# Performance work log

Measured on AMD Instinct MI355X. Metric: run time of the kernel, lower is better.

The kernel has to match this reference:

```python
import jax, jax.numpy as jnp
import numpy as np
import math

B, L, S, D = 4, 4096, 4096, 256
EPS = 1e-5

def _layernorm(x, g, b):
    mu = jnp.mean(x, axis=-1, keepdims=True)
    var = jnp.mean(jnp.square(x - mu), axis=-1, keepdims=True)
    return (x - mu) * jax.lax.rsqrt(var + EPS) * g + b

def setup_inputs() -> dict:
    key = jax.random.key(0)
    ks = jax.random.split(key, 14)
    s = 1.0 / math.sqrt(D)
    s2 = 1.0 / math.sqrt(2 * D)
    inp = {
        "source": jax.random.normal(ks[0], (B, L, D), jnp.float32),
        "target": jax.random.normal(ks[1], (B, S, D), jnp.float32),
        # linear weights stored as [in, out]
        "Wq": jax.random.uniform(ks[2], (D, D), jnp.float32, -s, s),
        "bq": jnp.zeros((D,), jnp.float32),
        "Wk": jax.random.uniform(ks[3], (D, D), jnp.float32, -s, s),
        "bk": jnp.zeros((D,), jnp.float32),
        "Wv": jax.random.uniform(ks[4], (D, D), jnp.float32, -s, s),
        "bv": jnp.zeros((D,), jnp.float32),
        "Wm": jax.random.uniform(ks[5], (D, D), jnp.float32, -s, s),
        "bm": jnp.zeros((D,), jnp.float32),
        "g1": jnp.ones((D,), jnp.float32),
        "beta1": jnp.zeros((D,), jnp.float32),
        "W1": jax.random.uniform(ks[6], (2 * D, 2 * D), jnp.float32, -s2, s2),
        "W2": jax.random.uniform(ks[7], (2 * D, D), jnp.float32, -s2, s2),
        "g2": jnp.ones((D,), jnp.float32),
        "beta2": jnp.zeros((D,), jnp.float32),
    }
    return inp

def reference(source, target, Wq, bq, Wk, bk, Wv, bv, Wm, bm, g1, beta1, W1, W2, g2, beta2):
    q = source @ Wq + bq              # [B, L, D]
    k = target @ Wk + bk              # [B, S, D]
    v = target @ Wv + bv              # [B, S, D]
    scale = 1.0 / math.sqrt(D)
    scores = jnp.einsum("bld,bsd->bls", q, k) * scale   # [B, L, S] materialized, as in source
    attn = jax.nn.softmax(scores, axis=-1)
    message = jnp.einsum("bls,bsd->bld", attn, v)        # [B, L, D]
    message = message @ Wm + bm
    message = _layernorm(message, g1, beta1)
    h = jnp.concatenate([source, message], axis=-1)      # [B, L, 2D]
    h = jax.nn.gelu(h @ W1, approximate=False)           # torch GELU is exact erf
    message = _layernorm(h @ W2, g2, beta2)
    return source + message
```

## Files before the change

### kernel.cpp

```cpp
#include <hip/hip_runtime.h>

typedef __bf16 bf16x8 __attribute__((ext_vector_type(8)));
typedef float f32x16 __attribute__((ext_vector_type(16)));
typedef float f32x4 __attribute__((ext_vector_type(4)));
typedef unsigned int u32;
typedef unsigned int u32x4 __attribute__((ext_vector_type(4)));
typedef unsigned short u16;
typedef unsigned short u16x4 __attribute__((ext_vector_type(4)));
typedef unsigned short u16x8 __attribute__((ext_vector_type(8)));

#define DEV static __device__ __forceinline__
#define AS1 __attribute__((address_space(1)))
#define AS3 __attribute__((address_space(3)))

DEV u16 f2bf(float f){
  unsigned u = __float_as_uint(f);
  u += 0x7FFFu + ((u >> 16) & 1u);
  return (u16)(u >> 16);
}
DEV float bf2f(u16 h){ return __uint_as_float(((u32)h) << 16); }

DEV void stage16(const u16* gsrc, const u16* ldst){
  __builtin_amdgcn_global_load_lds((const AS1 u32*)(unsigned long long)gsrc,
                                   (AS3 u32*)(u32)(unsigned long long)ldst,
                                   16, 0, 0);
}

constexpr int BATCH = 4, LQ = 4096, SK = 4096, DH = 256, BL = BATCH * LQ;
constexpr int NHALF = 2;
constexpr int ITERS = SK / NHALF / 64;

__global__ void prep_weights(const float* __restrict__ Wq, const float* __restrict__ Wk,
                             const float* __restrict__ Wv, const float* __restrict__ Wm,
                             const float* __restrict__ W1, const float* __restrict__ W2,
                             const float* __restrict__ bk, const float* __restrict__ bv,
                             u16* __restrict__ WqT, u16* __restrict__ WkvT,
                             u16* __restrict__ WmT,
                             u16* __restrict__ W1T, u16* __restrict__ W2T,
                             float* __restrict__ bkv){
  int idx = blockIdx.x * 256 + threadIdx.x;
  if (idx < 262144){
    int which = idx >> 16, i2 = idx & 65535;
    int r = i2 >> 8, c = i2 & 255;
    const float* S = (which==0)?Wq:(which==1)?Wk:(which==2)?Wv:Wm;
    u16*         D = (which==0)?WqT:(which==1)?WkvT:(which==2)?(WkvT+65536):WmT;
    D[c*256 + r] = f2bf(S[i2]);
  } else if (idx < 524288){
    int i2 = idx - 262144;
    int r = i2 >> 9, c = i2 & 511;
    W1T[c*512 + r] = f2bf(W1[i2]);
  } else if (idx < 655360){
    int i2 = idx - 524288;
    int r = i2 >> 8, c = i2 & 255;
    W2T[(size_t)c*512 + r] = f2bf(W2[i2]);
  } else if (idx < 655872){
    int i2 = idx - 655360;
    bkv[i2] = (i2 < 256) ? bk[i2] : bv[i2 - 256];
  }
}

__global__ __launch_bounds__(256, 2) void qkv_gemm(
  const float* __restrict__ src, const float* __restrict__ tgt,
  const u16* __restrict__ WqT, const u16* __restrict__ WkvT,
  const float* __restrict__ bq, const float* __restrict__ bkv,
  u16* __restrict__ qbuf, u16* __restrict__ kbuf, u16* __restrict__ vtbuf,
  u16* __restrict__ hcat, float qscale)
{
  __shared__ u16 A_lds[128 * 64];
  __shared__ u16 B_lds[128 * 64];
  const int tid = threadIdx.x, lane = tid & 63, wid = tid >> 6;
  const int ql = lane & 31, g = lane >> 5;
  const bool isQ = blockIdx.x < 2;
  const int m0 = blockIdx.y * 128;
  const int n0 = (isQ ? blockIdx.x : (blockIdx.x - 2)) * 128;
  const int mr = (wid & 1) * 64, nr = (wid >> 1) * 64;
  const float* Af = isQ ? src : tgt;
  const u16* BTp = isQ ? WqT : WkvT;
  const float* bias = isQ ? bq : bkv;
  const bool wh = isQ && (blockIdx.x == 0);

  f32x16 acc[2][2] = {};
  f32x4 afreg[8];
  u32x4 breg[4];

#define QK_LOAD_A(kb) do { \
    _Pragma("unroll") \
    for (int i = 0; i < 8; i++){ int item = tid + i*256; int r = item>>4, c = (item&15)*4; \
      afreg[i] = *(const f32x4*)&Af[(size_t)(m0+r)*256 + (kb)*64 + c]; } \
  } while(0)
#define QK_LOAD_B(kb) do { \
    _Pragma("unroll") \
    for (int i = 0; i < 4; i++){ int item = tid + i*256; int r = item>>3, c = (item&7)*8; \
      breg[i] = *(const u32x4*)&BTp[(size_t)(n0+r)*256 + (kb)*64 + c]; } \
  } while(0)

  QK_LOAD_A(0); QK_LOAD_B(0);

  for (int kb = 0; kb < 4; ++kb){
    __syncthreads();
    #pragma unroll
    for (int i = 0; i < 8; i++){ int item = tid + i*256; int r = item>>4, c = (item&15)*4;
      u16x4 h; h[0]=f2bf(afreg[i][0]); h[1]=f2bf(afreg[i][1]);
               h[2]=f2bf(afreg[i][2]); h[3]=f2bf(afreg[i][3]);
      *(u16x4*)&A_lds[r*64 + (c ^ ((r&7)*8))] = h;
      if (wh) *(u16x4*)&hcat[(size_t)(m0+r)*512 + kb*64 + c] = h;
    }
    #pragma unroll
    for (int i = 0; i < 4; i++){ int item = tid + i*256; int r = item>>3, c = (item&7)*8;
      *(u32x4*)&B_lds[r*64 + (c ^ ((r&7)*8))] = breg[i]; }
    __syncthreads();
    if (kb + 1 < 4){ QK_LOAD_A(kb+1); QK_LOAD_B(kb+1); }

    #pragma unroll
    for (int kk = 0; kk < 4; kk++){
      bf16x8 af[2], bf[2];
      #pragma unroll
      for (int mi = 0; mi < 2; mi++)
        af[mi] = __builtin_bit_cast(bf16x8,
          *(const u32x4*)&A_lds[(mr+mi*32+ql)*64 + ((kk*16+g*8) ^ ((ql&7)*8))]);
      #pragma unroll
      for (int ni = 0; ni < 2; ni++)
        bf[ni] = __builtin_bit_cast(bf16x8,
          *(const u32x4*)&B_lds[(nr+ni*32+ql)*64 + ((kk*16+g*8) ^ ((ql&7)*8))]);
      #pragma unroll
      for (int mi = 0; mi < 2; mi++)
        #pragma unroll
        for (int ni = 0; ni < 2; ni++)
          acc[mi][ni] = __builtin_amdgcn_mfma_f32_32x32x16_bf16(af[mi], bf[ni], acc[mi][ni], 0, 0, 0);
    }
  }

  #pragma unroll
  for (int mi = 0; mi < 2; mi++){
    #pragma unroll
    for (int ni = 0; ni < 2; ni++){
      const int col = n0 + nr + ni*32 + ql;
      const float bv = bias[col];
      if (isQ){
        #pragma unroll
        for (int j = 0; j < 16; j++){
          int row = m0 + mr + mi*32 + (j&3) + 8*(j>>2) + 4*g;
          qbuf[(size_t)row*256 + col] = f2bf((acc[mi][ni][j] + bv) * qscale);
        }
      } else if (col < 256){
        #pragma unroll
        for (int j = 0; j < 16; j++){
          int row = m0 + mr + mi*32 + (j&3) + 8*(j>>2) + 4*g;
          kbuf[(size_t)row*256 + col] = f2bf(acc[mi][ni][j] + bv);
        }
      } else {
        const int col2 = col - 256;
        #pragma unroll
        for (int qd = 0; qd < 4; qd++){
          u16x4 h;
          #pragma unroll
          for (int i = 0; i < 4; i++) h[i] = f2bf(acc[mi][ni][qd*4+i] + bv);
          int row0 = m0 + mr + mi*32 + qd*8 + 4*g;
          int bb = row0 >> 12, ss = row0 & 4095;
          *(u16x4*)&vtbuf[((size_t)bb*DH + col2)*SK + ss] = h;
        }
      }
    }
  }
}

__global__ __launch_bounds__(512, 2) void gemm_ln_wm(
  const u16* __restrict__ opart, const float* __restrict__ stats,
  const u16* __restrict__ BTp, const float* __restrict__ bias,
  const float* __restrict__ gamma, const float* __restrict__ beta,
  u16* __restrict__ outp)
{
  __shared__ __align__(16) char smem[65792];
  u16* A_lds = (u16*)smem;
  u16* B_lds = (u16*)(smem + 8192);
  float* scratch = (float*)smem;

  const int tid = threadIdx.x, lane = tid & 63, wid = tid >> 6;
  const int ql = lane & 31, g = lane >> 5;
  const int m0 = blockIdx.x * 64;
  const int ar = tid >> 3, ac = (tid & 7) * 8;

  float winv;
  { int row = m0 + ar;
    winv = 1.f / (stats[row] + stats[(size_t)BL + row]); }

  f32x16 acc[2] = {};
  u32x4 areg, areg2;
  u32x4 breg[4];

#define WM_LOAD_A(kb) do { \
    areg  = *(const u32x4*)&opart[(size_t)(m0+ar)*DH + (kb)*64 + ac]; \
    areg2 = *(const u32x4*)&opart[(size_t)BL*DH + (size_t)(m0+ar)*DH + (kb)*64 + ac]; \
  } while(0)
#define WM_LOAD_B(kb) do { \
    _Pragma("unroll") \
    for (int i = 0; i < 4; i++){ int item = tid + i*512; int r = item>>3, c = (item&7)*8; \
      breg[i] = *(const u32x4*)&BTp[(size_t)r*256 + (kb)*64 + c]; } \
  } while(0)

  WM_LOAD_A(0); WM_LOAD_B(0);

  for (int kb = 0; kb < 4; ++kb){
    __syncthreads();
    { u16x8 h;
      #pragma unroll
      for (int e = 0; e < 8; e++){
        u16 h0 = (u16)(areg[e>>1]  >> ((e&1)*16));
        u16 h1 = (u16)(areg2[e>>1] >> ((e&1)*16));
        h[e] = f2bf((bf2f(h0) + bf2f(h1)) * winv);
      }
      *(u16x8*)&A_lds[ar*64 + (ac ^ ((ar&7)*8))] = h; }
    #pragma unroll
    for (int i = 0; i < 4; i++){ int item = tid + i*512; int r = item>>3, c = (item&7)*8;
      *(u32x4*)&B_lds[r*64 + (c ^ ((r&7)*8))] = breg[i]; }
    __syncthreads();
    if (kb + 1 < 4){ WM_LOAD_A(kb+1); WM_LOAD_B(kb+1); }

    #pragma unroll
    for (int kk = 0; kk < 4; kk++){
      bf16x8 af[2];
      #pragma unroll
      for (int mi = 0; mi < 2; mi++)
        af[mi] = __builtin_bit_cast(bf16x8,
          *(const u32x4*)&A_lds[(mi*32+ql)*64 + ((kk*16+g*8) ^ ((ql&7)*8))]);
      bf16x8 bf = __builtin_bit_cast(bf16x8,
        *(const u32x4*)&B_lds[(wid*32+ql)*64 + ((kk*16+g*8) ^ ((ql&7)*8))]);
      #pragma unroll
      for (int mi = 0; mi < 2; mi++)
        acc[mi] = __builtin_amdgcn_mfma_f32_32x32x16_bf16(af[mi], bf, acc[mi], 0, 0, 0);
    }
  }

  __syncthreads();

  const float bv = bias[wid*32 + ql];
  #pragma unroll
  for (int mi = 0; mi < 2; mi++)
    #pragma unroll
    for (int j = 0; j < 16; j++){
      int row = mi*32 + (j&3) + 8*(j>>2) + 4*g;
      scratch[row*257 + wid*32 + ql] = acc[mi][j] + bv;
    }
  __syncthreads();

  f32x4 gv = *(const f32x4*)&gamma[lane*4];
  f32x4 bvv = *(const f32x4*)&beta[lane*4];
  #pragma unroll
  for (int rr = 0; rr < 8; rr++){
    const int row = wid*8 + rr;
    f32x4 v = *(const f32x4*)&scratch[row*257 + lane*4];
    float s1 = v[0]+v[1]+v[2]+v[3];
    float s2 = v[0]*v[0]+v[1]*v[1]+v[2]*v[2]+v[3]*v[3];
    #pragma unroll
    for (int m = 1; m < 64; m <<= 1){ s1 += __shfl_xor(s1, m, 64); s2 += __shfl_xor(s2, m, 64); }
    float mu = s1 * (1.f/DH);
    float var = s2 * (1.f/DH) - mu*mu;
    float rstd = rsqrtf(var + 1e-5f);
    u16x4 h;
    #pragma unroll
    for (int i = 0; i < 4; i++) h[i] = f2bf((v[i]-mu)*rstd*gv[i] + bvv[i]);
    *(u16x4*)&outp[(size_t)(m0+row)*512 + 256 + lane*4] = h;
  }
}

__global__ __launch_bounds__(512, 2) void fused_mlp(
  const u16* __restrict__ hcat, const u16* __restrict__ W1T,
  const u16* __restrict__ W2T, const float* __restrict__ gamma,
  const float* __restrict__ beta, const float* __restrict__ src,
  float* __restrict__ outp)
{
  __shared__ __align__(16) char smem[98304];
  u16* A1 = (u16*)smem;
  u16* B1 = (u16*)(smem + 8192);
  u16* Hl = (u16*)smem;
  u16* B2 = (u16*)(smem + 65536);
  float* scratch = (float*)smem;

  const int tid = threadIdx.x, lane = tid & 63, wid = tid >> 6;
  const int ql = lane & 31, g = lane >> 5;
  const int m0 = blockIdx.x * 64;

  f32x16 acc1[2][2] = {};
  for (int kb = 0; kb < 8; ++kb){
    if (kb) __syncthreads();
    { int r = tid >> 3, slot = tid & 7;
      stage16(&hcat[(size_t)(m0+r)*512 + kb*64 + ((slot ^ (r&7))<<3)],
              &A1[tid*8]); }
    #pragma unroll
    for (int i = 0; i < 8; i++){
      int grp = tid + i*512; int r = grp>>3, slot = grp&7;
      stage16(&W1T[(size_t)r*512 + kb*64 + ((slot ^ (r&7))<<3)], &B1[grp*8]);
    }
    __syncthreads();
    #pragma unroll
    for (int kk = 0; kk < 4; kk++){
      bf16x8 af[2];
      #pragma unroll
      for (int mi = 0; mi < 2; mi++)
        af[mi] = __builtin_bit_cast(bf16x8,
          *(const u32x4*)&A1[(mi*32+ql)*64 + ((kk*16+g*8) ^ ((ql&7)*8))]);
      #pragma unroll
      for (int ni = 0; ni < 2; ni++){
        int rB = wid*64 + ni*32 + ql;
        bf16x8 bf = __builtin_bit_cast(bf16x8,
          *(const u32x4*)&B1[rB*64 + ((kk*16+g*8) ^ ((ql&7)*8))]);
        #pragma unroll
        for (int mi = 0; mi < 2; mi++)
          acc1[mi][ni] = __builtin_amdgcn_mfma_f32_32x32x16_bf16(af[mi], bf, acc1[mi][ni], 0, 0, 0);
      }
    }
  }
  __syncthreads();

  #pragma unroll
  for (int mi = 0; mi < 2; mi++)
    #pragma unroll
    for (int ni = 0; ni < 2; ni++){
      const int col = wid*64 + ni*32 + ql;
      const int s = col >> 3;
      #pragma unroll
      for (int j = 0; j < 16; j++){
        int row = mi*32 + (j&3) + 8*(j>>2) + 4*g;
        float v = acc1[mi][ni][j];
        v = 0.5f * v * (1.f + erff(v * 0.70710678118f));
        Hl[row*512 + ((s ^ (row&7))<<3) + (col&7)] = f2bf(v);
      }
    }
  __syncthreads();

  f32x16 acc2[2] = {};
  for (int kb = 0; kb < 8; ++kb){
    if (kb) __syncthreads();
    #pragma unroll
    for (int i = 0; i < 4; i++){
      int grp = tid + i*512; int r = grp>>3, slot = grp&7;
      stage16(&W2T[(size_t)r*512 + kb*64 + ((slot ^ (r&7))<<3)], &B2[grp*8]);
    }
    __syncthreads();
    #pragma unroll
    for (int kk = 0; kk < 4; kk++){
      int c0s = (kb*64 + kk*16 + g*8) >> 3;
      bf16x8 af[2];
      #pragma unroll
      for (int mi = 0; mi < 2; mi++){
        int row = mi*32 + ql;
        af[mi] = __builtin_bit_cast(bf16x8,
          *(const u32x4*)&Hl[row*512 + ((c0s ^ (row&7))<<3)]);
      }
      bf16x8 bf = __builtin_bit_cast(bf16x8,
        *(const u32x4*)&B2[(wid*32+ql)*64 + ((kk*16+g*8) ^ ((ql&7)*8))]);
      #pragma unroll
      for (int mi = 0; mi < 2; mi++)
        acc2[mi] = __builtin_amdgcn_mfma_f32_32x32x16_bf16(af[mi], bf, acc2[mi], 0, 0, 0);
    }
  }
  __syncthreads();

  #pragma unroll
  for (int mi = 0; mi < 2; mi++)
    #pragma unroll
    for (int j = 0; j < 16; j++){
      int row = mi*32 + (j&3) + 8*(j>>2) + 4*g;
      scratch[row*257 + wid*32 + ql] = acc2[mi][j];
    }
  __syncthreads();

  f32x4 gv = *(const f32x4*)&gamma[lane*4];
  f32x4 bvv = *(const f32x4*)&beta[lane*4];
  #pragma unroll
  for (int rr = 0; rr < 8; rr++){
    const int row = wid*8 + rr;
    f32x4 v = *(const f32x4*)&scratch[row*257 + lane*4];
    float s1 = v[0]+v[1]+v[2]+v[3];
    float s2 = v[0]*v[0]+v[1]*v[1]+v[2]*v[2]+v[3]*v[3];
    #pragma unroll
    for (int m = 1; m < 64; m <<= 1){ s1 += __shfl_xor(s1, m, 64); s2 += __shfl_xor(s2, m, 64); }
    float mu = s1 * (1.f/DH);
    float var = s2 * (1.f/DH) - mu*mu;
    float rstd = rsqrtf(var + 1e-5f);
    f32x4 s = *(const f32x4*)&src[(size_t)(m0+row)*DH + lane*4];
    f32x4 o;
    #pragma unroll
    for (int i = 0; i < 4; i++) o[i] = s[i] + (v[i]-mu)*rstd*gv[i] + bvv[i];
    *(f32x4*)&outp[(size_t)(m0+row)*DH + lane*4] = o;
  }
}

__global__ __launch_bounds__(512, 2) void attn_kernel(
  const u16* __restrict__ qb, const u16* __restrict__ kb,
  const u16* __restrict__ vtb, u16* __restrict__ opart, float* __restrict__ stats)
{
  __shared__ u16 K_lds[2][64 * 256];
  __shared__ u16 VT_lds[2][256 * 64];
  __shared__ u32x4 P_exch[4][4][64];
  __shared__ float L_exch[4][2][32];

  const int tid = threadIdx.x;
  const int wid = tid >> 6, lane = tid & 63;
  const int ql = lane & 31, g = lane >> 5;
  const int qpair = wid >> 1, sh = wid & 1;
  const int b = blockIdx.y, half = blockIdx.z;
  const int qrow0 = blockIdx.x * 128 + qpair * 32;
  const int s0base = half * (SK / NHALF);

  const u16* kbase = kb  + (size_t)b * SK * DH;
  const u16* vbase = vtb + (size_t)b * DH * SK;

#define STAGE_K(bi, s0) do { \
    _Pragma("unroll") \
    for (int i = 0; i < 4; i++){ \
      int grp = tid + i*512; int s = grp>>5, slot = grp&31; \
      stage16(kbase + (size_t)((s0)+s)*DH + ((slot ^ (s&31))<<3), \
              &K_lds[bi][(i*512 + wid*64)*8]); \
    } } while(0)
#define STAGE_V(bi, s0) do { \
    _Pragma("unroll") \
    for (int i = 0; i < 4; i++){ \
      int grp = tid + i*512; int d = grp>>3, slot = grp&7; \
      stage16(vbase + (size_t)d*SK + (s0) + ((slot ^ (d&7))<<3), \
              &VT_lds[bi][(i*512 + wid*64)*8]); \
    } } while(0)

  STAGE_K(0, s0base);
  STAGE_V(0, s0base);

  bf16x8 qf[16];
  {
    const u16* qp = qb + ((size_t)(b*LQ + qrow0 + ql)) * DH + g * 8;
    #pragma unroll
    for (int kk = 0; kk < 16; kk++)
      qf[kk] = __builtin_bit_cast(bf16x8, *(const u32x4*)(qp + kk*16));
  }

  f32x16 accO[4] = {};
  float l_lane = 0.f;

  __syncthreads();

  for (int it = 0; it < ITERS; ++it){
    const int cur = it & 1;
    if (it + 1 < ITERS){
      STAGE_K(cur ^ 1, s0base + (it+1)*64);
      STAGE_V(cur ^ 1, s0base + (it+1)*64);
    }

    f32x16 ps = {};
    __builtin_amdgcn_s_setprio(1);
    #pragma unroll
    for (int kk = 0; kk < 16; ++kk){
      bf16x8 kf = __builtin_bit_cast(bf16x8,
        *(const u32x4*)&K_lds[cur][(sh*32+ql)*256 + (((kk*2+g) ^ ql)<<3)]);
      ps = __builtin_amdgcn_mfma_f32_32x32x16_bf16(kf, qf[kk], ps, 0, 0, 0);
    }
    __builtin_amdgcn_s_setprio(0);

    #pragma unroll
    for (int j = 0; j < 16; j++) ps[j] = exp2f(ps[j]);
    float s8[8];
    #pragma unroll
    for (int j = 0; j < 8; j++) s8[j] = ps[j] + ps[j+8];
    l_lane += ((s8[0]+s8[4]) + (s8[1]+s8[5])) + ((s8[2]+s8[6]) + (s8[3]+s8[7]));

    u32 Wp[4][2];
    #pragma unroll
    for (int qd = 0; qd < 4; qd++)
      #pragma unroll
      for (int h = 0; h < 2; h++){
        float lo = ps[qd*4 + 2*h], hi = ps[qd*4 + 2*h + 1];
        asm("v_cvt_pk_bf16_f32 %0, %1, %2" : "=v"(Wp[qd][h]) : "v"(lo), "v"(hi));
      }
    #pragma unroll
    for (int i = 0; i < 2; i++){
      const int qp2 = i * 2;
      u32 a0 = Wp[qp2][0], b0 = Wp[qp2+1][0];
      u32 a1 = Wp[qp2][1], b1 = Wp[qp2+1][1];
      asm("v_permlane32_swap_b32 %0, %1" : "+v"(a0), "+v"(b0));
      asm("v_permlane32_swap_b32 %0, %1" : "+v"(a1), "+v"(b1));
      u32x4 w; w[0] = a0; w[1] = a1; w[2] = b0; w[3] = b1;
      P_exch[qpair][sh*2 + i][lane] = w;
    }

    asm volatile("s_waitcnt lgkmcnt(0)" ::: "memory");
    __builtin_amdgcn_s_barrier();
    __builtin_amdgcn_sched_barrier(0);

    bf16x8 pf0 = __builtin_bit_cast(bf16x8, P_exch[qpair][0][lane]);
    bf16x8 pf1 = __builtin_bit_cast(bf16x8, P_exch[qpair][1][lane]);
    bf16x8 pf2 = __builtin_bit_cast(bf16x8, P_exch[qpair][2][lane]);
    bf16x8 pf3 = __builtin_bit_cast(bf16x8, P_exch[qpair][3][lane]);

    __builtin_amdgcn_s_setprio(1);
    #pragma unroll
    for (int dt = 0; dt < 4; dt++){
      const int dtg = sh*4 + dt;
      bf16x8 vf0 = __builtin_bit_cast(bf16x8,
        *(const u32x4*)&VT_lds[cur][(dtg*32+ql)*64 + (((0*2+g) ^ (ql&7))<<3)]);
      accO[dt] = __builtin_amdgcn_mfma_f32_32x32x16_bf16(vf0, pf0, accO[dt], 0, 0, 0);
      bf16x8 vf1 = __builtin_bit_cast(bf16x8,
        *(const u32x4*)&VT_lds[cur][(dtg*32+ql)*64 + (((1*2+g) ^ (ql&7))<<3)]);
      accO[dt] = __builtin_amdgcn_mfma_f32_32x32x16_bf16(vf1, pf1, accO[dt], 0, 0, 0);
      bf16x8 vf2 = __builtin_bit_cast(bf16x8,
        *(const u32x4*)&VT_lds[cur][(dtg*32+ql)*64 + (((2*2+g) ^ (ql&7))<<3)]);
      accO[dt] = __builtin_amdgcn_mfma_f32_32x32x16_bf16(vf2, pf2, accO[dt], 0, 0, 0);
      bf16x8 vf3 = __builtin_bit_cast(bf16x8,
        *(const u32x4*)&VT_lds[cur][(dtg*32+ql)*64 + (((3*2+g) ^ (ql&7))<<3)]);
      accO[dt] = __builtin_amdgcn_mfma_f32_32x32x16_bf16(vf3, pf3, accO[dt], 0, 0, 0);
    }
    __builtin_amdgcn_s_setprio(0);

    asm volatile("s_waitcnt vmcnt(0) lgkmcnt(0)" ::: "memory");
    __builtin_amdgcn_s_barrier();
    __builtin_amdgcn_sched_barrier(0);
  }

  float l_run = l_lane + __shfl_xor(l_lane, 32, 64);
  if (g == 0) L_exch[qpair][sh][ql] = l_run;
  __syncthreads();
  float l_tot = l_run + L_exch[qpair][sh^1][ql];

  const int rowb = b * LQ + qrow0;
  if (sh == 0 && g == 0)
    stats[(size_t)half*BL + rowb + ql] = l_tot;

  float* scratch = (float*)&K_lds[0][0] + wid * 1056;
  #pragma unroll
  for (int dt = 0; dt < 4; dt++){
    const int dtg = sh*4 + dt;
    #pragma unroll
    for (int j = 0; j < 16; j++){
      int dl = (j&3) + 8*(j>>2) + 4*g;
      scratch[ql*33 + dl] = accO[dt][j];
    }
    int q2 = lane >> 1, dl2 = (lane & 1) * 16;
    u16x8 h0, h1;
    #pragma unroll
    for (int i = 0; i < 8; i++){ h0[i] = f2bf(scratch[q2*33 + dl2 + i]);
                                 h1[i] = f2bf(scratch[q2*33 + dl2 + 8 + i]); }
    u16* op = &opart[((size_t)half*BL + rowb + q2)*DH + dtg*32 + dl2];
    *(u16x8*)op = h0;
    *(u16x8*)(op + 8) = h1;
  }
}

extern "C" void kernel_launch(void* const* d_in, const int* in_sizes, int n_in,
                              void* d_out, int out_size, void* d_ws, size_t ws_size,
                              hipStream_t stream)
{
  const float* source = (const float*)d_in[0];
  const float* target = (const float*)d_in[1];
  const float* Wq = (const float*)d_in[2];  const float* bq = (const float*)d_in[3];
  const float* Wk = (const float*)d_in[4];  const float* bk = (const float*)d_in[5];
  const float* Wv = (const float*)d_in[6];  const float* bv = (const float*)d_in[7];
  const float* Wm = (const float*)d_in[8];  const float* bm = (const float*)d_in[9];
  const float* g1 = (const float*)d_in[10]; const float* be1 = (const float*)d_in[11];
  const float* W1 = (const float*)d_in[12]; const float* W2 = (const float*)d_in[13];
  const float* g2 = (const float*)d_in[14]; const float* be2 = (const float*)d_in[15];

  char* ws = (char*)d_ws;
  u16* WqT  = (u16*)(ws);
  u16* WkvT = (u16*)(ws + (size_t)(1u<<17));
  u16* WmT  = (u16*)(ws + (size_t)3*(1u<<17));
  u16* W1T  = (u16*)(ws + (size_t)4*(1u<<17));
  u16* W2T  = (u16*)(ws + (size_t)8*(1u<<17));
  float* bkv = (float*)(ws + (size_t)10*(1u<<17));
  size_t off = (size_t)10*(1u<<17) + 4096;
  u16* qbuf  = (u16*)(ws + off); off += (size_t)BL*DH*2;
  u16* kbuf  = (u16*)(ws + off); off += (size_t)BL*DH*2;
  u16* vtbuf = (u16*)(ws + off); off += (size_t)BL*DH*2;
  u16* hcat  = (u16*)(ws + off); off += (size_t)BL*512*2;
  u16* opart = (u16*)(ws + off); off += (size_t)NHALF*BL*DH*2;
  float* stats = (float*)(ws + off); off += (size_t)NHALF*BL*4;

  prep_weights<<<dim3(2562), 256, 0, stream>>>(Wq, Wk, Wv, Wm, W1, W2, bk, bv,
                                               WqT, WkvT, WmT, W1T, W2T, bkv);

  const float qscale = 1.4426950408889634f / 16.0f;
  qkv_gemm<<<dim3(6, BL/128), 256, 0, stream>>>(
      source, target, WqT, WkvT, bq, bkv, qbuf, kbuf, vtbuf, hcat, qscale);

  attn_kernel<<<dim3(LQ/128, BATCH, NHALF), 512, 0, stream>>>(qbuf, kbuf, vtbuf, opart, stats);

  gemm_ln_wm<<<dim3(BL/64), 512, 0, stream>>>(opart, stats, WmT, bm, g1, be1, hcat);

  fused_mlp<<<dim3(BL/64), 512, 0, stream>>>(hcat, W1T, W2T, g2, be2, source,
                                             (float*)d_out);
}
```

Before: 160.6 us.

## Retile QKV GEMM to full-width rows and overlap own-half PV before barrier

The QKV projection now gives each block 64 rows and a full 256-wide output slice per path (Q, K or V), using 512 threads with 8 waves each owning 32 columns. Each source/target row tile is converted once per path instead of being split across column blocks, and the hcat copy is written as 8-wide vectors. In attention, each wave now runs the PV MFMAs for its own half of the P tile straight from registers before the barrier, and reads only the partner half from LDS afterwards. This is meant to hide barrier latency behind matrix work. The cost is a different B-tile footprint and grid shape in the GEMM, plus some register pressure from keeping pfo live.

```diff
diff --git a/kernel.cpp b/kernel.cpp
--- a/kernel.cpp
+++ b/kernel.cpp
@@ -59,108 +59,93 @@
   }
 }
 
-__global__ __launch_bounds__(256, 2) void qkv_gemm(
+__global__ __launch_bounds__(512, 2) void qkv_gemm(
   const float* __restrict__ src, const float* __restrict__ tgt,
   const u16* __restrict__ WqT, const u16* __restrict__ WkvT,
   const float* __restrict__ bq, const float* __restrict__ bkv,
   u16* __restrict__ qbuf, u16* __restrict__ kbuf, u16* __restrict__ vtbuf,
   u16* __restrict__ hcat, float qscale)
 {
-  __shared__ u16 A_lds[128 * 64];
-  __shared__ u16 B_lds[128 * 64];
+  __shared__ u16 A_lds[64 * 64];
+  __shared__ u16 B_lds[256 * 64];
   const int tid = threadIdx.x, lane = tid & 63, wid = tid >> 6;
   const int ql = lane & 31, g = lane >> 5;
-  const bool isQ = blockIdx.x < 2;
-  const int m0 = blockIdx.y * 128;
-  const int n0 = (isQ ? blockIdx.x : (blockIdx.x - 2)) * 128;
-  const int mr = (wid & 1) * 64, nr = (wid >> 1) * 64;
-  const float* Af = isQ ? src : tgt;
-  const u16* BTp = isQ ? WqT : WkvT;
-  const float* bias = isQ ? bq : bkv;
-  const bool wh = isQ && (blockIdx.x == 0);
-
-  f32x16 acc[2][2] = {};
-  f32x4 afreg[8];
+  const int path = blockIdx.x;
+  const int m0 = blockIdx.y * 64;
+  const float* Af = (path == 0) ? src : tgt;
+  const u16* BTp = (path == 0) ? WqT : (WkvT + (size_t)(path - 1) * 65536);
+  const float* bias = (path == 0) ? bq : (bkv + (path - 1) * 256);
+  const int ar = tid >> 3, ac = (tid & 7) * 8;
+
+  f32x16 acc[2] = {};
+  f32x4 af0, af1;
   u32x4 breg[4];
 
-#define QK_LOAD_A(kb) do { \
+#define QKV_LOAD_A(kb) do { \
+    af0 = *(const f32x4*)&Af[(size_t)(m0+ar)*256 + (kb)*64 + ac]; \
+    af1 = *(const f32x4*)&Af[(size_t)(m0+ar)*256 + (kb)*64 + ac + 4]; \
+  } while(0)
+#define QKV_LOAD_B(kb) do { \
     _Pragma("unroll") \
-    for (int i = 0; i < 8; i++){ int item = tid + i*256; int r = item>>4, c = (item&15)*4; \
-      afreg[i] = *(const f32x4*)&Af[(size_t)(m0+r)*256 + (kb)*64 + c]; } \
+    for (int i = 0; i < 4; i++){ int item = tid + i*512; int r = item>>3, c = (item&7)*8; \
+      breg[i] = *(const u32x4*)&BTp[(size_t)r*256 + (kb)*64 + c]; } \
   } while(0)
-#define QK_LOAD_B(kb) do { \
-    _Pragma("unroll") \
-    for (int i = 0; i < 4; i++){ int item = tid + i*256; int r = item>>3, c = (item&7)*8; \
-      breg[i] = *(const u32x4*)&BTp[(size_t)(n0+r)*256 + (kb)*64 + c]; } \
-  } while(0)
-
-  QK_LOAD_A(0); QK_LOAD_B(0);
+
+  QKV_LOAD_A(0); QKV_LOAD_B(0);
 
   for (int kb = 0; kb < 4; ++kb){
     __syncthreads();
-    #pragma unroll
-    for (int i = 0; i < 8; i++){ int item = tid + i*256; int r = item>>4, c = (item&15)*4;
-      u16x4 h; h[0]=f2bf(afreg[i][0]); h[1]=f2bf(afreg[i][1]);
-               h[2]=f2bf(afreg[i][2]); h[3]=f2bf(afreg[i][3]);
-      *(u16x4*)&A_lds[r*64 + (c ^ ((r&7)*8))] = h;
-      if (wh) *(u16x4*)&hcat[(size_t)(m0+r)*512 + kb*64 + c] = h;
-    }
-    #pragma unroll
-    for (int i = 0; i < 4; i++){ int item = tid + i*256; int r = item>>3, c = (item&7)*8;
+    { u16x8 h;
+      h[0]=f2bf(af0[0]); h[1]=f2bf(af0[1]); h[2]=f2bf(af0[2]); h[3]=f2bf(af0[3]);
+      h[4]=f2bf(af1[0]); h[5]=f2bf(af1[1]); h[6]=f2bf(af1[2]); h[7]=f2bf(af1[3]);
+      *(u16x8*)&A_lds[ar*64 + (ac ^ ((ar&7)*8))] = h;
+      if (path == 0) *(u16x8*)&hcat[(size_t)(m0+ar)*512 + kb*64 + ac] = h;
+    }
+    #pragma unroll
+    for (int i = 0; i < 4; i++){ int item = tid + i*512; int r = item>>3, c = (item&7)*8;
       *(u32x4*)&B_lds[r*64 + (c ^ ((r&7)*8))] = breg[i]; }
     __syncthreads();
-    if (kb + 1 < 4){ QK_LOAD_A(kb+1); QK_LOAD_B(kb+1); }
+    if (kb + 1 < 4){ QKV_LOAD_A(kb+1); QKV_LOAD_B(kb+1); }
 
     #pragma unroll
     for (int kk = 0; kk < 4; kk++){
-      bf16x8 af[2], bf[2];
+      bf16x8 af[2];
       #pragma unroll
       for (int mi = 0; mi < 2; mi++)
         af[mi] = __builtin_bit_cast(bf16x8,
-          *(const u32x4*)&A_lds[(mr+mi*32+ql)*64 + ((kk*16+g*8) ^ ((ql&7)*8))]);
-      #pragma unroll
-      for (int ni = 0; ni < 2; ni++)
-        bf[ni] = __builtin_bit_cast(bf16x8,
-          *(const u32x4*)&B_lds[(nr+ni*32+ql)*64 + ((kk*16+g*8) ^ ((ql&7)*8))]);
+          *(const u32x4*)&A_lds[(mi*32+ql)*64 + ((kk*16+g*8) ^ ((ql&7)*8))]);
+      bf16x8 bf = __builtin_bit_cast(bf16x8,
+        *(const u32x4*)&B_lds[(wid*32+ql)*64 + ((kk*16+g*8) ^ ((ql&7)*8))]);
       #pragma unroll
       for (int mi = 0; mi < 2; mi++)
+        acc[mi] = __builtin_amdgcn_mfma_f32_32x32x16_bf16(af[mi], bf, acc[mi], 0, 0, 0);
+    }
+  }
+
+  const int col = wid*32 + ql;
+  const float bv = bias[col];
+  if (path == 2){
+    #pragma unroll
+    for (int mi = 0; mi < 2; mi++)
+      #pragma unroll
+      for (int qd = 0; qd < 4; qd++){
+        u16x4 h;
         #pragma unroll
-        for (int ni = 0; ni < 2; ni++)
-          acc[mi][ni] = __builtin_amdgcn_mfma_f32_32x32x16_bf16(af[mi], bf[ni], acc[mi][ni], 0, 0, 0);
-    }
-  }
-
-  #pragma unroll
-  for (int mi = 0; mi < 2; mi++){
-    #pragma unroll
-    for (int ni = 0; ni < 2; ni++){
-      const int col = n0 + nr + ni*32 + ql;
-      const float bv = bias[col];
-      if (isQ){
-        #pragma unroll
-        for (int j = 0; j < 16; j++){
-          int row = m0 + mr + mi*32 + (j&3) + 8*(j>>2) + 4*g;
-          qbuf[(size_t)row*256 + col] = f2bf((acc[mi][ni][j] + bv) * qscale);
-        }
-      } else if (col < 256){
-        #pragma unroll
-        for (int j = 0; j < 16; j++){
-          int row = m0 + mr + mi*32 + (j&3) + 8*(j>>2) + 4*g;
-          kbuf[(size_t)row*256 + col] = f2bf(acc[mi][ni][j] + bv);
-        }
-      } else {
-        const int col2 = col - 256;
-        #pragma unroll
-        for (int qd = 0; qd < 4; qd++){
-          u16x4 h;
-          #pragma unroll
-          for (int i = 0; i < 4; i++) h[i] = f2bf(acc[mi][ni][qd*4+i] + bv);
-          int row0 = m0 + mr + mi*32 + qd*8 + 4*g;
-          int bb = row0 >> 12, ss = row0 & 4095;
-          *(u16x4*)&vtbuf[((size_t)bb*DH + col2)*SK + ss] = h;
-        }
-      }
-    }
+        for (int i = 0; i < 4; i++) h[i] = f2bf(acc[mi][qd*4+i] + bv);
+        int row0 = m0 + mi*32 + qd*8 + 4*g;
+        int bb = row0 >> 12, ss = row0 & 4095;
+        *(u16x4*)&vtbuf[((size_t)bb*DH + col)*SK + ss] = h;
+      }
+  } else {
+    u16* outp = (path == 0) ? qbuf : kbuf;
+    const float sc = (path == 0) ? qscale : 1.0f;
+    #pragma unroll
+    for (int mi = 0; mi < 2; mi++)
+      #pragma unroll
+      for (int j = 0; j < 16; j++){
+        int row = m0 + mi*32 + (j&3) + 8*(j>>2) + 4*g;
+        outp[(size_t)row*256 + col] = f2bf((acc[mi][j] + bv) * sc);
+      }
   }
 }
 
@@ -456,10 +441,6 @@
 
     #pragma unroll
     for (int j = 0; j < 16; j++) ps[j] = exp2f(ps[j]);
-    float s8[8];
-    #pragma unroll
-    for (int j = 0; j < 8; j++) s8[j] = ps[j] + ps[j+8];
-    l_lane += ((s8[0]+s8[4]) + (s8[1]+s8[5])) + ((s8[2]+s8[6]) + (s8[3]+s8[7]));
 
     u32 Wp[4][2];
     #pragma unroll
@@ -469,6 +450,7 @@
         float lo = ps[qd*4 + 2*h], hi = ps[qd*4 + 2*h + 1];
         asm("v_cvt_pk_bf16_f32 %0, %1, %2" : "=v"(Wp[qd][h]) : "v"(lo), "v"(hi));
       }
+    bf16x8 pfo[2];
     #pragma unroll
     for (int i = 0; i < 2; i++){
       const int qp2 = i * 2;
@@ -478,33 +460,46 @@
       asm("v_permlane32_swap_b32 %0, %1" : "+v"(a1), "+v"(b1));
       u32x4 w; w[0] = a0; w[1] = a1; w[2] = b0; w[3] = b1;
       P_exch[qpair][sh*2 + i][lane] = w;
-    }
+      pfo[i] = __builtin_bit_cast(bf16x8, w);
+    }
+
+    __builtin_amdgcn_s_setprio(1);
+    #pragma unroll
+    for (int dt = 0; dt < 4; dt++){
+      const int dtg = sh*4 + dt;
+      const int k0 = sh*2;
+      bf16x8 vf0 = __builtin_bit_cast(bf16x8,
+        *(const u32x4*)&VT_lds[cur][(dtg*32+ql)*64 + ((((k0+0)*2+g) ^ (ql&7))<<3)]);
+      accO[dt] = __builtin_amdgcn_mfma_f32_32x32x16_bf16(vf0, pfo[0], accO[dt], 0, 0, 0);
+      bf16x8 vf1 = __builtin_bit_cast(bf16x8,
+        *(const u32x4*)&VT_lds[cur][(dtg*32+ql)*64 + ((((k0+1)*2+g) ^ (ql&7))<<3)]);
+      accO[dt] = __builtin_amdgcn_mfma_f32_32x32x16_bf16(vf1, pfo[1], accO[dt], 0, 0, 0);
+    }
+    __builtin_amdgcn_s_setprio(0);
+
+    { float s8[8];
+      #pragma unroll
+      for (int j = 0; j < 8; j++) s8[j] = ps[j] + ps[j+8];
+      l_lane += ((s8[0]+s8[4]) + (s8[1]+s8[5])) + ((s8[2]+s8[6]) + (s8[3]+s8[7])); }
 
     asm volatile("s_waitcnt lgkmcnt(0)" ::: "memory");
     __builtin_amdgcn_s_barrier();
     __builtin_amdgcn_sched_barrier(0);
 
-    bf16x8 pf0 = __builtin_bit_cast(bf16x8, P_exch[qpair][0][lane]);
-    bf16x8 pf1 = __builtin_bit_cast(bf16x8, P_exch[qpair][1][lane]);
-    bf16x8 pf2 = __builtin_bit_cast(bf16x8, P_exch[qpair][2][lane]);
-    bf16x8 pf3 = __builtin_bit_cast(bf16x8, P_exch[qpair][3][lane]);
+    bf16x8 pfp0 = __builtin_bit_cast(bf16x8, P_exch[qpair][(sh^1)*2 + 0][lane]);
+    bf16x8 pfp1 = __builtin_bit_cast(bf16x8, P_exch[qpair][(sh^1)*2 + 1][lane]);
 
     __builtin_amdgcn_s_setprio(1);
     #pragma unroll
     for (int dt = 0; dt < 4; dt++){
       const int dtg = sh*4 + dt;
+      const int k0 = (sh^1)*2;
       bf16x8 vf0 = __builtin_bit_cast(bf16x8,
-        *(const u32x4*)&VT_lds[cur][(dtg*32+ql)*64 + (((0*2+g) ^ (ql&7))<<3)]);
-      accO[dt] = __builtin_amdgcn_mfma_f32_32x32x16_bf16(vf0, pf0, accO[dt], 0, 0, 0);
+        *(const u32x4*)&VT_lds[cur][(dtg*32+ql)*64 + ((((k0+0)*2+g) ^ (ql&7))<<3)]);
+      accO[dt] = __builtin_amdgcn_mfma_f32_32x32x16_bf16(vf0, pfp0, accO[dt], 0, 0, 0);
       bf16x8 vf1 = __builtin_bit_cast(bf16x8,
-        *(const u32x4*)&VT_lds[cur][(dtg*32+ql)*64 + (((1*2+g) ^ (ql&7))<<3)]);
-      accO[dt] = __builtin_amdgcn_mfma_f32_32x32x16_bf16(vf1, pf1, accO[dt], 0, 0, 0);
-      bf16x8 vf2 = __builtin_bit_cast(bf16x8,
-        *(const u32x4*)&VT_lds[cur][(dtg*32+ql)*64 + (((2*2+g) ^ (ql&7))<<3)]);
-      accO[dt] = __builtin_amdgcn_mfma_f32_32x32x16_bf16(vf2, pf2, accO[dt], 0, 0, 0);
-      bf16x8 vf3 = __builtin_bit_cast(bf16x8,
-        *(const u32x4*)&VT_lds[cur][(dtg*32+ql)*64 + (((3*2+g) ^ (ql&7))<<3)]);
-      accO[dt] = __builtin_amdgcn_mfma_f32_32x32x16_bf16(vf3, pf3, accO[dt], 0, 0, 0);
+        *(const u32x4*)&VT_lds[cur][(dtg*32+ql)*64 + ((((k0+1)*2+g) ^ (ql&7))<<3)]);
+      accO[dt] = __builtin_amdgcn_mfma_f32_32x32x16_bf16(vf1, pfp1, accO[dt], 0, 0, 0);
     }
     __builtin_amdgcn_s_setprio(0);
 
@@ -575,7 +570,7 @@
                                                WqT, WkvT, WmT, W1T, W2T, bkv);
 
   const float qscale = 1.4426950408889634f / 16.0f;
-  qkv_gemm<<<dim3(6, BL/128), 256, 0, stream>>>(
+  qkv_gemm<<<dim3(3, BL/64), 512, 0, stream>>>(
       source, target, WqT, WkvT, bq, bkv, qbuf, kbuf, vtbuf, hcat, qscale);
 
   attn_kernel<<<dim3(LQ/128, BATCH, NHALF), 512, 0, stream>>>(qbuf, kbuf, vtbuf, opart, stats);
```

After: 153.0 us. -4.8%, faster.
